# Kernel optimization log

Hardware: AMD Instinct MI355X
Metric: run time of the kernel (lower is better)

Reference implementation:

```python
import jax, jax.numpy as jnp
import numpy as np

# Module hyperparameters (from init_kwargs)
N_S = 128                      # n_scalars
L2_IDX = (0, 1, 2, 3, 4, 5, 6) # l2_indices
N_L2 = len(L2_IDX) + 1         # selected l=2 kernels + their sum -> 8
H = 256                        # hidden multiplicity
B = 2048                       # batch
K = 8                          # number of kernels in kernel_t2s


def _w3j_222():
    """Real-basis Wigner 3j for (2e,2e)->2e, Frobenius norm 1 (e3nn convention).
    Built as tr(Qa Qb Qc) over an orthonormal basis of symmetric traceless 3x3
    matrices (the unique invariant 3-tensor on the 5-dim l=2 irrep)."""
    Q = np.zeros((5, 3, 3))
    s = 1.0 / np.sqrt(2.0)
    Q[0, 0, 1] = Q[0, 1, 0] = s
    Q[1, 1, 2] = Q[1, 2, 1] = s
    Q[2] = np.diag([-1.0, -1.0, 2.0]) / np.sqrt(6.0)
    Q[3, 0, 2] = Q[3, 2, 0] = s
    Q[4, 0, 0] = s
    Q[4, 1, 1] = -s
    C = np.einsum('aij,bjk,cki->abc', Q, Q, Q)
    return C / np.linalg.norm(C)

C222 = jnp.asarray(_w3j_222(), dtype=jnp.float32)

# e3nn FullyConnectedTensorProduct path normalization ('component'/'element'):
# coeff = sqrt((2*l_out+1) / sum over paths into same output of mul1*mul2)
C0 = float(np.sqrt(1.0 / (N_S**2 + N_L2**2)))            # paths into Hx0e: 0x0->0, 2x2->0
C2 = float(np.sqrt(5.0 / (2 * N_S * N_L2 + N_L2**2)))    # paths into Hx2e: 0x2, 2x0, 2x2
C2B = float(np.sqrt(5.0 / (3 * H**2)))                   # tp2 paths into 1x2e
INV_S5 = float(1.0 / np.sqrt(5.0))                       # w3j(l,l,0) = I/sqrt(2l+1), l=2


def setup_inputs() -> dict:
    key = jax.random.key(0)
    ks = jax.random.split(key, 10)
    f32 = jnp.float32
    return {
        'scalars': jax.random.normal(ks[0], (B, N_S), f32),
        'kernel_t2s': jax.random.normal(ks[1], (B, K, 5), f32),
        'W000': jax.random.normal(ks[2], (N_S, N_S, H), f32),
        'W220': jax.random.normal(ks[3], (N_L2, N_L2, H), f32),
        'W022': jax.random.normal(ks[4], (N_S, N_L2, H), f32),
        'W202': jax.random.normal(ks[5], (N_L2, N_S, H), f32),
        'W222': jax.random.normal(ks[6], (N_L2, N_L2, H), f32),
        'V022': jax.random.normal(ks[7], (H, H, 1), f32),
        'V202': jax.random.normal(ks[8], (H, H, 1), f32),
        'V222': jax.random.normal(ks[9], (H, H, 1), f32),
    }


def reference(scalars, kernel_t2s, W000, W220, W022, W202, W222, V022, V202, V222):
    ee = lambda *a: jnp.einsum(*a, optimize='optimal')
    idx = jnp.asarray(L2_IDX)
    # build tp input: [B, n_s] scalars  ++  [B, n_l2, 5] l=2 features
    t = jnp.concatenate([kernel_t2s[:, idx, :],
                         kernel_t2s.sum(axis=1, keepdims=True)], axis=1)  # [B, N_L2, 5]
    s = scalars                                                            # [B, N_S]

    # tp1(x, x): Hx0e + Hx2e
    y0 = C0 * (ee('uvw,zu,zv->zw', W000, s, s)
               + INV_S5 * ee('uvw,zui,zvi->zw', W220, t, t))               # [B, H]
    y2 = C2 * (INV_S5 * (ee('uvw,zu,zvk->zwk', W022, s, t)
                         + ee('uvw,zuk,zv->zwk', W202, t, s))
               + ee('uvw,ijk,zui,zvj->zwk', W222, C222, t, t))             # [B, H, 5]

    # tp2(y, y): 1x2e
    out = C2B * (INV_S5 * (ee('uvw,zu,zvk->zwk', V022, y0, y2)
                           + ee('uvw,zuk,zv->zwk', V202, y2, y0))
                 + ee('uvw,ijk,zui,zvj->zwk', V222, C222, y2, y2))         # [B, 1, 5]
    return out[:, 0, :]                                                    # [B, 5]
```

## Files before the change

### kernel.cpp

```cpp
#include <hip/hip_runtime.h>
#include <stdint.h>
#include <stddef.h>


#define NS     128
#define NL2    8
#define HH     256
#define NB     2048

#define KPAIR  8256
#define KPAD   8448
#define GLEN   64
#define KSPLIT 16
#define CHUNK  528
#define KT     16
#define NTILES 33

#define C0F  0.00779729f
#define C2F  0.04865619f
#define C2BF 0.005042948f
#define IS5  0.44721360f

constexpr size_t OFF_C222 = 0;
constexpr size_t OFF_PU   = 128;
constexpr size_t OFF_PV   = 8576;
constexpr size_t OFF_T    = 17024;
constexpr size_t OFF_W222 = 98944;
constexpr size_t OFF_VBS  = 115328;
constexpr size_t OFF_VC   = 180864;
constexpr size_t OFF_ST   = 246400;
constexpr size_t OFF_GT   = 508544;
constexpr size_t OFF_Y0   = 639616;
constexpr size_t OFF_ACP  = 1163904;
constexpr size_t WS_FLOATS = 1688192;

#define SEG_T    81920
#define SEG_PUV  90368
#define SEG_W222 106752
#define SEG_VBS  172288
#define SEG_VC   237824
#define SEG_ST   499968
#define SEG_GT   631040
#define SEG_END  1155328

__global__ __launch_bounds__(256) void prep_k(
    const float* __restrict__ scalars, const float* __restrict__ kt2s,
    const float* __restrict__ W222,
    const float* __restrict__ V022, const float* __restrict__ V202,
    const float* __restrict__ V222, float* __restrict__ ws) {
  const int tid = threadIdx.x;

  if (blockIdx.x == 0) {
    __shared__ float cv[125];
    __shared__ float inv;
    float val = 0.f;
    if (tid < 125) {
      float Q[45];
      #pragma unroll
      for (int q = 0; q < 45; ++q) Q[q] = 0.f;
      const float s2 = 0.70710678f, s6 = 0.40824829f;
      Q[0*9+0*3+1] = s2;  Q[0*9+1*3+0] = s2;
      Q[1*9+1*3+2] = s2;  Q[1*9+2*3+1] = s2;
      Q[2*9+0*3+0] = -s6; Q[2*9+1*3+1] = -s6; Q[2*9+2*3+2] = 2.f*s6;
      Q[3*9+0*3+2] = s2;  Q[3*9+2*3+0] = s2;
      Q[4*9+0*3+0] = s2;  Q[4*9+1*3+1] = -s2;
      const int a = tid/25, b = (tid/5)%5, c = tid%5;
      for (int i = 0; i < 3; ++i)
        for (int j = 0; j < 3; ++j)
          for (int k = 0; k < 3; ++k)
            val += Q[a*9+i*3+j]*Q[b*9+j*3+k]*Q[c*9+k*3+i];
      cv[tid] = val;
    }
    __syncthreads();
    if (tid == 0) {
      float sq = 0.f;
      for (int p = 0; p < 125; ++p) sq += cv[p]*cv[p];
      inv = 1.0f/sqrtf(sq);
    }
    __syncthreads();
    if (tid < 125) ws[OFF_C222 + tid] = val*inv;
    return;
  }

  int* pu = (int*)(ws + OFF_PU);
  int* pv = (int*)(ws + OFF_PV);
  const int stride = (gridDim.x - 1)*256;
  for (int i = (blockIdx.x - 1)*256 + tid; i < SEG_END; i += stride) {
    if (i < SEG_T) {
      int z = i/40, r = i - z*40, u = r/5, ii = r - u*5;
      float v;
      if (u < 7) v = kt2s[z*40 + u*5 + ii];
      else {
        v = 0.f;
        for (int k = 0; k < 8; ++k) v += kt2s[z*40 + k*5 + ii];
      }
      ws[OFF_T + i] = v;
    } else if (i < SEG_PUV) {
      int p = i - SEG_T;
      int u = 0, vv = 0;
      if (p < KPAIR) {
        int rem = p;
        while (rem >= NS - u) { rem -= NS - u; ++u; }
        vv = u + rem;
      } else if (p < KPAIR + 36) {
        int q = p - KPAIR;
        while (q >= NL2 - u) { q -= NL2 - u; ++u; }
        vv = u + q;
      }
      pu[p] = u; pv[p] = vv;
    } else if (i < SEG_W222) {
      int j = i - SEG_PUV;
      ws[OFF_W222 + j] = C2F*W222[j];
    } else if (i < SEG_VBS) {
      int j = i - SEG_W222;
      int u = j >> 8, c = j & 255;
      ws[OFF_VBS + j] = (C2BF*IS5)*(V022[u*HH + c] + V202[c*HH + u]);
    } else if (i < SEG_VC) {
      int j = i - SEG_VBS;
      ws[OFF_VC + j] = C2BF*V222[j];
    } else if (i < SEG_ST) {
      int j = i - SEG_VC;
      int u = j >> 11, z = j & 2047;
      ws[OFF_ST + j] = scalars[(size_t)z*NS + u];
    } else if (i < SEG_GT) {
      int j = i - SEG_ST;
      int q = j >> 11, z = j & 2047;
      float v = 0.f;
      if (q < 36) {
        int qq = q, u = 0;
        while (qq >= NL2 - u) { qq -= NL2 - u; ++u; }
        int vv = u + qq;
        const float* kz = kt2s + (size_t)z*40;
        #pragma unroll
        for (int ii = 0; ii < 5; ++ii) {
          float tu, tv;
          if (u < 7) tu = kz[u*5 + ii];
          else { tu = 0.f; for (int k = 0; k < 8; ++k) tu += kz[k*5 + ii]; }
          if (vv < 7) tv = kz[vv*5 + ii];
          else { tv = 0.f; for (int k = 0; k < 8; ++k) tv += kz[k*5 + ii]; }
          v += tu*tv;
        }
      }
      ws[OFF_GT + j] = v;
    } else {
      ws[OFF_Y0 + (i - SEG_GT)] = 0.f;
    }
  }
}

__global__ __launch_bounds__(256, 4) void gemm_y0_k(
    const float* __restrict__ W000, const float* __restrict__ W220,
    float* __restrict__ ws) {
  const int* pu = (const int*)(ws + OFF_PU);
  const int* pv = (const int*)(ws + OFF_PV);
  const float* sT = ws + OFF_ST;
  const float* gT = ws + OFF_GT;
  float* y0 = ws + OFF_Y0;

  __shared__ __align__(16) float As[2][KT][64];
  __shared__ __align__(16) float Bs[2][KT][128];

  const int tid = threadIdx.x;
  const int bid = blockIdx.x;
  const int ks = bid & 15, mtnt = bid >> 4;
  const int mt = mtnt >> 1, nt = mtnt & 1;
  const int z0 = mt*64, n0 = nt*128;
  const int kbase = ks*CHUNK;
  const int m = tid & 63, w = tid >> 6;
  const int tx = tid & 31, ty = tid >> 5;

  float4 bReg[2];
  float  aReg[4];

  auto load_tile = [&](int t) {
    const int k0 = kbase + t*KT;
    #pragma unroll
    for (int e = 0; e < 2; ++e) {
      int idx = e*256 + tid;
      int r = idx >> 5, col = (idx & 31)*4;
      int p = k0 + r;
      float4 val;
      if (p < KPAIR) {
        int u = pu[p], v = pv[p];
        float4 a = *reinterpret_cast<const float4*>(
            &W000[((size_t)u*NS + v)*HH + n0 + col]);
        if (u != v) {
          float4 b = *reinterpret_cast<const float4*>(
              &W000[((size_t)v*NS + u)*HH + n0 + col]);
          val = make_float4(C0F*(a.x+b.x), C0F*(a.y+b.y),
                            C0F*(a.z+b.z), C0F*(a.w+b.w));
        } else {
          val = make_float4(C0F*a.x, C0F*a.y, C0F*a.z, C0F*a.w);
        }
      } else if (p < KPAIR + 36) {
        int u = pu[p], v = pv[p];
        const float sc = C0F*IS5;
        float4 a = *reinterpret_cast<const float4*>(
            &W220[(u*NL2 + v)*HH + n0 + col]);
        if (u != v) {
          float4 b = *reinterpret_cast<const float4*>(
              &W220[(v*NL2 + u)*HH + n0 + col]);
          val = make_float4(sc*(a.x+b.x), sc*(a.y+b.y),
                            sc*(a.z+b.z), sc*(a.w+b.w));
        } else {
          val = make_float4(sc*a.x, sc*a.y, sc*a.z, sc*a.w);
        }
      } else {
        val = make_float4(0.f, 0.f, 0.f, 0.f);
      }
      bReg[e] = val;
    }
    #pragma unroll
    for (int e = 0; e < 4; ++e) {
      int k = k0 + e*4 + w;
      float a;
      if (k < KPAIR) {
        a = sT[(size_t)pu[k]*NB + z0 + m] * sT[(size_t)pv[k]*NB + z0 + m];
      } else {
        int q = k - KPAIR;
        a = (q < GLEN) ? gT[(size_t)q*NB + z0 + m] : 0.f;
      }
      aReg[e] = a;
    }
  };
  auto store_tile = [&](int buf) {
    #pragma unroll
    for (int e = 0; e < 2; ++e) {
      int idx = e*256 + tid;
      int r = idx >> 5, col = (idx & 31)*4;
      *reinterpret_cast<float4*>(&Bs[buf][r][col]) = bReg[e];
    }
    #pragma unroll
    for (int e = 0; e < 4; ++e) As[buf][e*4 + w][m] = aReg[e];
  };

  float acc[8][4];
  #pragma unroll
  for (int i = 0; i < 8; ++i)
    #pragma unroll
    for (int j = 0; j < 4; ++j) acc[i][j] = 0.f;

  load_tile(0);
  store_tile(0);
  __syncthreads();

  for (int t = 0; t < NTILES; ++t) {
    if (t + 1 < NTILES) load_tile(t + 1);
    const int cur = t & 1;
    #pragma unroll
    for (int kk = 0; kk < KT; ++kk) {
      float4 a0 = *reinterpret_cast<const float4*>(&As[cur][kk][ty*8]);
      float4 a1 = *reinterpret_cast<const float4*>(&As[cur][kk][ty*8+4]);
      float4 bv = *reinterpret_cast<const float4*>(&Bs[cur][kk][tx*4]);
      float am[8] = {a0.x,a0.y,a0.z,a0.w,a1.x,a1.y,a1.z,a1.w};
      float bn[4] = {bv.x,bv.y,bv.z,bv.w};
      #pragma unroll
      for (int mi = 0; mi < 8; ++mi)
        #pragma unroll
        for (int ni = 0; ni < 4; ++ni)
          acc[mi][ni] += am[mi]*bn[ni];
    }
    if (t + 1 < NTILES) store_tile(cur ^ 1);
    __syncthreads();
  }

  #pragma unroll
  for (int mi = 0; mi < 8; ++mi) {
    int z = z0 + ty*8 + mi;
    #pragma unroll
    for (int ni = 0; ni < 4; ++ni)
      atomicAdd(&y0[(size_t)z*HH + n0 + tx*4 + ni], acc[mi][ni]);
  }
}

__global__ __launch_bounds__(256) void gemm_rm_k(
    const float* __restrict__ A, const float* __restrict__ B,
    float* __restrict__ C, int M, int N, int K) {
  __shared__ __align__(16) float As[32][68];
  __shared__ __align__(16) float Bs[32][68];
  const int tid = threadIdx.x, tx = tid & 15, ty = tid >> 4;
  const int n0 = blockIdx.x*64, m0 = blockIdx.y*64;
  float acc[4][4];
  #pragma unroll
  for (int i = 0; i < 4; ++i)
    #pragma unroll
    for (int j = 0; j < 4; ++j) acc[i][j] = 0.f;

  for (int k0 = 0; k0 < K; k0 += 32) {
    __syncthreads();
    #pragma unroll
    for (int e = 0; e < 2; ++e) {
      int r = e*32 + (tid >> 3);
      int kc = (tid & 7)*4;
      float4 v = *reinterpret_cast<const float4*>(&A[(size_t)(m0+r)*K + k0 + kc]);
      As[kc+0][r] = v.x; As[kc+1][r] = v.y; As[kc+2][r] = v.z; As[kc+3][r] = v.w;
    }
    #pragma unroll
    for (int e = 0; e < 2; ++e) {
      int idx = e*256 + tid;
      int r = idx >> 4, c4 = idx & 15;
      float4 v = *reinterpret_cast<const float4*>(&B[(size_t)(k0+r)*N + n0 + c4*4]);
      *reinterpret_cast<float4*>(&Bs[r][c4*4]) = v;
    }
    __syncthreads();
    #pragma unroll
    for (int kk = 0; kk < 32; ++kk) {
      float4 av = *reinterpret_cast<const float4*>(&As[kk][ty*4]);
      float4 bv = *reinterpret_cast<const float4*>(&Bs[kk][tx*4]);
      float am[4] = {av.x, av.y, av.z, av.w};
      float bn[4] = {bv.x, bv.y, bv.z, bv.w};
      #pragma unroll
      for (int i = 0; i < 4; ++i)
        #pragma unroll
        for (int j = 0; j < 4; ++j) acc[i][j] += am[i]*bn[j];
    }
  }
  #pragma unroll
  for (int i = 0; i < 4; ++i) {
    float4 v = make_float4(acc[i][0], acc[i][1], acc[i][2], acc[i][3]);
    *reinterpret_cast<float4*>(&C[(size_t)(m0 + ty*4 + i)*N + n0 + tx*4]) = v;
  }
}

__global__ __launch_bounds__(256) void mega_k(
    const float* __restrict__ scalars, const float* __restrict__ W022,
    const float* __restrict__ W202, const float* __restrict__ ws,
    float* __restrict__ out) {
  const float* tg    = ws + OFF_T;
  const float* W222c = ws + OFF_W222;
  const float* VC    = ws + OFF_VC;
  const float* acp   = ws + OFF_ACP;
  const float* c222g = ws + OFF_C222;

  __shared__ float ts[8][40];
  __shared__ float c2s[125];
  __shared__ __align__(16) float sb[8][128];
  __shared__ __align__(16) float ovl[10240];
  float* tC  = ovl;
  float* RsF = ovl + 1600;
  float* y2s = ovl;

  const int tid = threadIdx.x;
  const int zg0 = blockIdx.x*8;
  const int lane = tid & 63, wv = tid >> 6;

  if (tid < 125) c2s[tid] = c222g[tid];
  for (int r = tid; r < 320; r += 256) {
    int z = r/40, c = r - z*40;
    ts[z][c] = tg[(size_t)(zg0 + z)*40 + c];
  }
  {
    int z = tid >> 5, c4 = tid & 31;
    float4 v = reinterpret_cast<const float4*>(scalars + (size_t)(zg0 + z)*NS)[c4];
    sb[z][c4*4+0] = v.x; sb[z][c4*4+1] = v.y;
    sb[z][c4*4+2] = v.z; sb[z][c4*4+3] = v.w;
  }
  __syncthreads();

  for (int idx = tid; idx < 1600; idx += 256) {
    int z = idx/200, r = idx - z*200, v = r/25, ik = r - v*25;
    int i = ik/5, k = ik - i*5;
    float a = 0.f;
    #pragma unroll
    for (int j = 0; j < 5; ++j) a += c2s[(i*5+j)*5 + k]*ts[z][v*5+j];
    tC[idx] = a;
  }
  __syncthreads();
  for (int idx = tid; idx < 2560; idx += 256) {
    int uv = idx/40, r = idx - uv*40, z = r/5, k = r - z*5;
    int u = uv >> 3, v = uv & 7;
    float a = 0.f;
    #pragma unroll
    for (int ii = 0; ii < 5; ++ii) a += ts[z][u*5+ii]*tC[z*200 + v*25 + ii*5 + k];
    RsF[idx] = a;
  }
  __syncthreads();

  float acc[8][5];
  #pragma unroll
  for (int z = 0; z < 8; ++z)
    #pragma unroll
    for (int k = 0; k < 5; ++k) acc[z][k] = 0.f;

  for (int vg = 0; vg < 4; ++vg) {
    float av[4][8];
    #pragma unroll
    for (int vi = 0; vi < 4; ++vi)
      #pragma unroll
      for (int z = 0; z < 8; ++z) av[vi][z] = 0.f;
    for (int u4 = 0; u4 < 128; u4 += 4) {
      float4 szv[8];
      #pragma unroll
      for (int z = 0; z < 8; ++z) szv[z] = *reinterpret_cast<const float4*>(&sb[z][u4]);
      #pragma unroll
      for (int uu = 0; uu < 4; ++uu) {
        int u = u4 + uu;
        #pragma unroll
        for (int vi = 0; vi < 4; ++vi) {
          float w1v = (vg < 2)
            ? W022[((size_t)u*NL2 + (vg*4+vi))*HH + tid]
            : W202[((size_t)((vg-2)*4+vi)*NS + u)*HH + tid];
          #pragma unroll
          for (int z = 0; z < 8; ++z) {
            float su = (uu==0)?szv[z].x:(uu==1)?szv[z].y:(uu==2)?szv[z].z:szv[z].w;
            av[vi][z] += su*w1v;
          }
        }
      }
    }
    #pragma unroll
    for (int vi = 0; vi < 4; ++vi) {
      int vmap = (vg*4 + vi) & 7;
      #pragma unroll
      for (int z = 0; z < 8; ++z) {
        float avs = (C2F*IS5)*av[vi][z];
        #pragma unroll
        for (int k = 0; k < 5; ++k)
          acc[z][k] += avs*ts[z][vmap*5+k];
      }
    }
  }

  for (int uv = 0; uv < 64; ++uv) {
    float wvv = W222c[uv*256 + tid];
    #pragma unroll
    for (int c4 = 0; c4 < 10; ++c4) {
      float4 rv = *reinterpret_cast<const float4*>(&RsF[uv*40 + c4*4]);
      acc[(c4*4+0)/5][(c4*4+0)%5] += wvv*rv.x;
      acc[(c4*4+1)/5][(c4*4+1)%5] += wvv*rv.y;
      acc[(c4*4+2)/5][(c4*4+2)%5] += wvv*rv.z;
      acc[(c4*4+3)/5][(c4*4+3)%5] += wvv*rv.w;
    }
  }

  __syncthreads();
  #pragma unroll
  for (int z = 0; z < 8; ++z)
    #pragma unroll
    for (int k = 0; k < 5; ++k)
      y2s[z*1280 + k*256 + tid] = acc[z][k];
  __syncthreads();

  float hacc[2][5][4];
  #pragma unroll
  for (int zz = 0; zz < 2; ++zz)
    #pragma unroll
    for (int i = 0; i < 5; ++i)
      #pragma unroll
      for (int j = 0; j < 4; ++j) hacc[zz][i][j] = 0.f;

  for (int u4 = 0; u4 < 256; u4 += 4) {
    float vc[4][4];
    #pragma unroll
    for (int uu = 0; uu < 4; ++uu)
      #pragma unroll
      for (int j = 0; j < 4; ++j)
        vc[uu][j] = VC[(size_t)(u4+uu)*256 + lane + 64*j];
    #pragma unroll
    for (int zz = 0; zz < 2; ++zz) {
      int z = wv*2 + zz;
      #pragma unroll
      for (int i = 0; i < 5; ++i) {
        float4 yv = *reinterpret_cast<const float4*>(&y2s[z*1280 + i*256 + u4]);
        float ya[4] = {yv.x, yv.y, yv.z, yv.w};
        #pragma unroll
        for (int uu = 0; uu < 4; ++uu)
          #pragma unroll
          for (int j = 0; j < 4; ++j)
            hacc[zz][i][j] += ya[uu]*vc[uu][j];
      }
    }
  }

  float outp[2][5];
  #pragma unroll
  for (int zz = 0; zz < 2; ++zz)
    #pragma unroll
    for (int k = 0; k < 5; ++k) outp[zz][k] = 0.f;

  for (int j = 0; j < 4; ++j) {
    int v = lane + 64*j;
    #pragma unroll
    for (int zz = 0; zz < 2; ++zz) {
      int z = wv*2 + zz;
      float y2v[5];
      #pragma unroll
      for (int jp = 0; jp < 5; ++jp) y2v[jp] = y2s[z*1280 + jp*256 + v];
      float avv = acp[(size_t)(zg0 + z)*256 + v];
      #pragma unroll
      for (int k = 0; k < 5; ++k) outp[zz][k] += avv*y2v[k];
      #pragma unroll
      for (int i = 0; i < 5; ++i) {
        float hv = hacc[zz][i][j];
        #pragma unroll
        for (int jp = 0; jp < 5; ++jp) {
          float pj = hv*y2v[jp];
          #pragma unroll
          for (int k = 0; k < 5; ++k)
            outp[zz][k] += pj*c2s[i*25 + jp*5 + k];
        }
      }
    }
  }

  #pragma unroll
  for (int zz = 0; zz < 2; ++zz)
    #pragma unroll
    for (int k = 0; k < 5; ++k) {
      float vsum = outp[zz][k];
      #pragma unroll
      for (int off = 32; off > 0; off >>= 1) vsum += __shfl_xor(vsum, off, 64);
      if (lane == 0) out[(size_t)(zg0 + wv*2 + zz)*5 + k] = vsum;
    }
}

extern "C" void kernel_launch(void* const* d_in, const int* in_sizes, int n_in,
                              void* d_out, int out_size, void* d_ws, size_t ws_size,
                              hipStream_t stream) {
  (void)in_sizes; (void)n_in; (void)out_size;
  const float* scalars = (const float*)d_in[0];
  const float* kt2s    = (const float*)d_in[1];
  const float* W000    = (const float*)d_in[2];
  const float* W220    = (const float*)d_in[3];
  const float* W022    = (const float*)d_in[4];
  const float* W202    = (const float*)d_in[5];
  const float* W222    = (const float*)d_in[6];
  const float* V022    = (const float*)d_in[7];
  const float* V202    = (const float*)d_in[8];
  const float* V222    = (const float*)d_in[9];
  float* out = (float*)d_out;
  float* ws  = (float*)d_ws;
  if (ws_size < WS_FLOATS*sizeof(float)) return;

  prep_k<<<1025, 256, 0, stream>>>(scalars, kt2s, W222, V022, V202, V222, ws);
  gemm_y0_k<<<1024, 256, 0, stream>>>(W000, W220, ws);
  gemm_rm_k<<<dim3(4, 32), 256, 0, stream>>>(ws + OFF_Y0, ws + OFF_VBS,
                                             (float*)(ws + OFF_ACP), 2048, 256, 256);
  mega_k<<<256, 256, 0, stream>>>(scalars, W022, W202, ws, out);
}
```

Baseline: 498.1 us.

## Widen y0 GEMM tile, precombine W022/W202, and split mega kernel finer

gemm_y0_k now has each block cover the full 256-wide output with an 8x8 per-thread tile. This halves the block count and stops gathering the pair-product A operand twice, once per N tile. prep_k now writes a combined, prescaled W022+W202 tensor, so mega_k reads one weight stream for the 0x2 and 2x0 paths. mega_k handles 2 batch rows per block instead of 8, launching 1024 blocks instead of 256. Its final contraction reduces 30 partial sums per wave through shuffles and shared memory. The costs are more register pressure in the GEMM (64 accumulators, occupancy hint dropped), a larger workspace, and more total weight traffic in mega_k because fewer rows share each weight load.

```diff
diff --git a/kernel.cpp b/kernel.cpp
--- a/kernel.cpp
+++ b/kernel.cpp
@@ -9,7 +9,6 @@
 #define NB     2048
 
 #define KPAIR  8256
-#define KPAD   8448
 #define GLEN   64
 #define KSPLIT 16
 #define CHUNK  528
@@ -30,9 +29,10 @@
 constexpr size_t OFF_VC   = 180864;
 constexpr size_t OFF_ST   = 246400;
 constexpr size_t OFF_GT   = 508544;
-constexpr size_t OFF_Y0   = 639616;
-constexpr size_t OFF_ACP  = 1163904;
-constexpr size_t WS_FLOATS = 1688192;
+constexpr size_t OFF_WC2  = 639616;
+constexpr size_t OFF_Y0   = 901760;
+constexpr size_t OFF_ACP  = 1426048;
+constexpr size_t WS_FLOATS = 1950336;
 
 #define SEG_T    81920
 #define SEG_PUV  90368
@@ -41,10 +41,12 @@
 #define SEG_VC   237824
 #define SEG_ST   499968
 #define SEG_GT   631040
-#define SEG_END  1155328
+#define SEG_WC2  893184
+#define SEG_END  1417472
 
 __global__ __launch_bounds__(256) void prep_k(
     const float* __restrict__ scalars, const float* __restrict__ kt2s,
+    const float* __restrict__ W022, const float* __restrict__ W202,
     const float* __restrict__ W222,
     const float* __restrict__ V022, const float* __restrict__ V202,
     const float* __restrict__ V222, float* __restrict__ ws) {
@@ -142,13 +144,18 @@
         }
       }
       ws[OFF_GT + j] = v;
+    } else if (i < SEG_WC2) {
+      int j = i - SEG_GT;
+      int u = j >> 11, r = j & 2047, v = r >> 8, w = r & 255;
+      ws[OFF_WC2 + j] = (C2F*IS5)*(W022[((size_t)u*NL2 + v)*HH + w]
+                                   + W202[((size_t)v*NS + u)*HH + w]);
     } else {
-      ws[OFF_Y0 + (i - SEG_GT)] = 0.f;
+      ws[OFF_Y0 + (i - SEG_WC2)] = 0.f;
     }
   }
 }
 
-__global__ __launch_bounds__(256, 4) void gemm_y0_k(
+__global__ __launch_bounds__(256) void gemm_y0_k(
     const float* __restrict__ W000, const float* __restrict__ W220,
     float* __restrict__ ws) {
   const int* pu = (const int*)(ws + OFF_PU);
@@ -158,35 +165,34 @@
   float* y0 = ws + OFF_Y0;
 
   __shared__ __align__(16) float As[2][KT][64];
-  __shared__ __align__(16) float Bs[2][KT][128];
+  __shared__ __align__(16) float Bs[2][KT][256];
 
   const int tid = threadIdx.x;
   const int bid = blockIdx.x;
-  const int ks = bid & 15, mtnt = bid >> 4;
-  const int mt = mtnt >> 1, nt = mtnt & 1;
-  const int z0 = mt*64, n0 = nt*128;
+  const int ks = bid & 15, mt = bid >> 4;
+  const int z0 = mt*64;
   const int kbase = ks*CHUNK;
   const int m = tid & 63, w = tid >> 6;
   const int tx = tid & 31, ty = tid >> 5;
 
-  float4 bReg[2];
+  float4 bReg[4];
   float  aReg[4];
 
   auto load_tile = [&](int t) {
     const int k0 = kbase + t*KT;
     #pragma unroll
-    for (int e = 0; e < 2; ++e) {
-      int idx = e*256 + tid;
-      int r = idx >> 5, col = (idx & 31)*4;
+    for (int e = 0; e < 4; ++e) {
+      int r = e*4 + w;
+      int col = (tid & 63)*4;
       int p = k0 + r;
       float4 val;
       if (p < KPAIR) {
         int u = pu[p], v = pv[p];
         float4 a = *reinterpret_cast<const float4*>(
-            &W000[((size_t)u*NS + v)*HH + n0 + col]);
+            &W000[((size_t)u*NS + v)*HH + col]);
         if (u != v) {
           float4 b = *reinterpret_cast<const float4*>(
-              &W000[((size_t)v*NS + u)*HH + n0 + col]);
+              &W000[((size_t)v*NS + u)*HH + col]);
           val = make_float4(C0F*(a.x+b.x), C0F*(a.y+b.y),
                             C0F*(a.z+b.z), C0F*(a.w+b.w));
         } else {
@@ -196,10 +202,10 @@
         int u = pu[p], v = pv[p];
         const float sc = C0F*IS5;
         float4 a = *reinterpret_cast<const float4*>(
-            &W220[(u*NL2 + v)*HH + n0 + col]);
+            &W220[(u*NL2 + v)*HH + col]);
         if (u != v) {
           float4 b = *reinterpret_cast<const float4*>(
-              &W220[(v*NL2 + u)*HH + n0 + col]);
+              &W220[(v*NL2 + u)*HH + col]);
           val = make_float4(sc*(a.x+b.x), sc*(a.y+b.y),
                             sc*(a.z+b.z), sc*(a.w+b.w));
         } else {
@@ -225,20 +231,20 @@
   };
   auto store_tile = [&](int buf) {
     #pragma unroll
-    for (int e = 0; e < 2; ++e) {
-      int idx = e*256 + tid;
-      int r = idx >> 5, col = (idx & 31)*4;
+    for (int e = 0; e < 4; ++e) {
+      int r = e*4 + w;
+      int col = (tid & 63)*4;
       *reinterpret_cast<float4*>(&Bs[buf][r][col]) = bReg[e];
     }
     #pragma unroll
     for (int e = 0; e < 4; ++e) As[buf][e*4 + w][m] = aReg[e];
   };
 
-  float acc[8][4];
+  float acc[8][8];
   #pragma unroll
   for (int i = 0; i < 8; ++i)
     #pragma unroll
-    for (int j = 0; j < 4; ++j) acc[i][j] = 0.f;
+    for (int j = 0; j < 8; ++j) acc[i][j] = 0.f;
 
   load_tile(0);
   store_tile(0);
@@ -251,13 +257,14 @@
     for (int kk = 0; kk < KT; ++kk) {
       float4 a0 = *reinterpret_cast<const float4*>(&As[cur][kk][ty*8]);
       float4 a1 = *reinterpret_cast<const float4*>(&As[cur][kk][ty*8+4]);
-      float4 bv = *reinterpret_cast<const float4*>(&Bs[cur][kk][tx*4]);
+      float4 b0 = *reinterpret_cast<const float4*>(&Bs[cur][kk][tx*8]);
+      float4 b1 = *reinterpret_cast<const float4*>(&Bs[cur][kk][tx*8+4]);
       float am[8] = {a0.x,a0.y,a0.z,a0.w,a1.x,a1.y,a1.z,a1.w};
-      float bn[4] = {bv.x,bv.y,bv.z,bv.w};
+      float bn[8] = {b0.x,b0.y,b0.z,b0.w,b1.x,b1.y,b1.z,b1.w};
       #pragma unroll
       for (int mi = 0; mi < 8; ++mi)
         #pragma unroll
-        for (int ni = 0; ni < 4; ++ni)
+        for (int ni = 0; ni < 8; ++ni)
           acc[mi][ni] += am[mi]*bn[ni];
     }
     if (t + 1 < NTILES) store_tile(cur ^ 1);
@@ -268,8 +275,8 @@
   for (int mi = 0; mi < 8; ++mi) {
     int z = z0 + ty*8 + mi;
     #pragma unroll
-    for (int ni = 0; ni < 4; ++ni)
-      atomicAdd(&y0[(size_t)z*HH + n0 + tx*4 + ni], acc[mi][ni]);
+    for (int ni = 0; ni < 8; ++ni)
+      atomicAdd(&y0[(size_t)z*HH + tx*8 + ni], acc[mi][ni]);
   }
 }
 
@@ -323,33 +330,33 @@
 }
 
 __global__ __launch_bounds__(256) void mega_k(
-    const float* __restrict__ scalars, const float* __restrict__ W022,
-    const float* __restrict__ W202, const float* __restrict__ ws,
+    const float* __restrict__ scalars, const float* __restrict__ ws,
     float* __restrict__ out) {
   const float* tg    = ws + OFF_T;
+  const float* WC2   = ws + OFF_WC2;
   const float* W222c = ws + OFF_W222;
   const float* VC    = ws + OFF_VC;
   const float* acp   = ws + OFF_ACP;
   const float* c222g = ws + OFF_C222;
 
-  __shared__ float ts[8][40];
+  __shared__ float ts[2][40];
   __shared__ float c2s[125];
-  __shared__ __align__(16) float sb[8][128];
-  __shared__ __align__(16) float ovl[10240];
-  float* tC  = ovl;
-  float* RsF = ovl + 1600;
-  float* y2s = ovl;
+  __shared__ float sb[2][128];
+  __shared__ float tC[2][200];
+  __shared__ float Rs[2][320];
+  __shared__ float y2s[2][1280];
+  __shared__ float Pl[4][30];
 
   const int tid = threadIdx.x;
-  const int zg0 = blockIdx.x*8;
+  const int zg0 = blockIdx.x*2;
   const int lane = tid & 63, wv = tid >> 6;
 
   if (tid < 125) c2s[tid] = c222g[tid];
-  for (int r = tid; r < 320; r += 256) {
-    int z = r/40, c = r - z*40;
+  if (tid < 80) {
+    int z = tid/40, c = tid - (tid/40)*40;
     ts[z][c] = tg[(size_t)(zg0 + z)*40 + c];
   }
-  {
+  if (tid < 64) {
     int z = tid >> 5, c4 = tid & 31;
     float4 v = reinterpret_cast<const float4*>(scalars + (size_t)(zg0 + z)*NS)[c4];
     sb[z][c4*4+0] = v.x; sb[z][c4*4+1] = v.y;
@@ -357,161 +364,116 @@
   }
   __syncthreads();
 
-  for (int idx = tid; idx < 1600; idx += 256) {
+  for (int idx = tid; idx < 400; idx += 256) {
     int z = idx/200, r = idx - z*200, v = r/25, ik = r - v*25;
     int i = ik/5, k = ik - i*5;
     float a = 0.f;
     #pragma unroll
     for (int j = 0; j < 5; ++j) a += c2s[(i*5+j)*5 + k]*ts[z][v*5+j];
-    tC[idx] = a;
+    tC[z][r] = a;
   }
   __syncthreads();
-  for (int idx = tid; idx < 2560; idx += 256) {
-    int uv = idx/40, r = idx - uv*40, z = r/5, k = r - z*5;
+  for (int idx = tid; idx < 640; idx += 256) {
+    int z = idx/320, r = idx - (idx/320)*320, uv = r/5, k = r - uv*5;
     int u = uv >> 3, v = uv & 7;
     float a = 0.f;
     #pragma unroll
-    for (int ii = 0; ii < 5; ++ii) a += ts[z][u*5+ii]*tC[z*200 + v*25 + ii*5 + k];
-    RsF[idx] = a;
+    for (int ii = 0; ii < 5; ++ii) a += ts[z][u*5+ii]*tC[z][v*25 + ii*5 + k];
+    Rs[z][r] = a;
   }
   __syncthreads();
 
-  float acc[8][5];
-  #pragma unroll
-  for (int z = 0; z < 8; ++z)
+  float acc[2][5];
+  #pragma unroll
+  for (int z = 0; z < 2; ++z)
     #pragma unroll
     for (int k = 0; k < 5; ++k) acc[z][k] = 0.f;
 
-  for (int vg = 0; vg < 4; ++vg) {
-    float av[4][8];
-    #pragma unroll
-    for (int vi = 0; vi < 4; ++vi)
-      #pragma unroll
-      for (int z = 0; z < 8; ++z) av[vi][z] = 0.f;
-    for (int u4 = 0; u4 < 128; u4 += 4) {
-      float4 szv[8];
-      #pragma unroll
-      for (int z = 0; z < 8; ++z) szv[z] = *reinterpret_cast<const float4*>(&sb[z][u4]);
-      #pragma unroll
-      for (int uu = 0; uu < 4; ++uu) {
-        int u = u4 + uu;
-        #pragma unroll
-        for (int vi = 0; vi < 4; ++vi) {
-          float w1v = (vg < 2)
-            ? W022[((size_t)u*NL2 + (vg*4+vi))*HH + tid]
-            : W202[((size_t)((vg-2)*4+vi)*NS + u)*HH + tid];
-          #pragma unroll
-          for (int z = 0; z < 8; ++z) {
-            float su = (uu==0)?szv[z].x:(uu==1)?szv[z].y:(uu==2)?szv[z].z:szv[z].w;
-            av[vi][z] += su*w1v;
-          }
-        }
-      }
-    }
-    #pragma unroll
-    for (int vi = 0; vi < 4; ++vi) {
-      int vmap = (vg*4 + vi) & 7;
-      #pragma unroll
-      for (int z = 0; z < 8; ++z) {
-        float avs = (C2F*IS5)*av[vi][z];
-        #pragma unroll
-        for (int k = 0; k < 5; ++k)
-          acc[z][k] += avs*ts[z][vmap*5+k];
-      }
-    }
-  }
-
+  #pragma unroll 2
+  for (int v = 0; v < 8; ++v) {
+    float av0 = 0.f, av1 = 0.f;
+    const float* wp = WC2 + v*256 + tid;
+    #pragma unroll 4
+    for (int u = 0; u < 128; ++u) {
+      float wcv = wp[(size_t)u*2048];
+      av0 += sb[0][u]*wcv;
+      av1 += sb[1][u]*wcv;
+    }
+    #pragma unroll
+    for (int k = 0; k < 5; ++k) {
+      acc[0][k] += av0*ts[0][v*5+k];
+      acc[1][k] += av1*ts[1][v*5+k];
+    }
+  }
   for (int uv = 0; uv < 64; ++uv) {
     float wvv = W222c[uv*256 + tid];
     #pragma unroll
-    for (int c4 = 0; c4 < 10; ++c4) {
-      float4 rv = *reinterpret_cast<const float4*>(&RsF[uv*40 + c4*4]);
-      acc[(c4*4+0)/5][(c4*4+0)%5] += wvv*rv.x;
-      acc[(c4*4+1)/5][(c4*4+1)%5] += wvv*rv.y;
-      acc[(c4*4+2)/5][(c4*4+2)%5] += wvv*rv.z;
-      acc[(c4*4+3)/5][(c4*4+3)%5] += wvv*rv.w;
-    }
-  }
-
+    for (int z = 0; z < 2; ++z)
+      #pragma unroll
+      for (int k = 0; k < 5; ++k)
+        acc[z][k] += wvv*Rs[z][uv*5 + k];
+  }
+  #pragma unroll
+  for (int z = 0; z < 2; ++z)
+    #pragma unroll
+    for (int k = 0; k < 5; ++k)
+      y2s[z][k*256 + tid] = acc[z][k];
   __syncthreads();
-  #pragma unroll
-  for (int z = 0; z < 8; ++z)
-    #pragma unroll
-    for (int k = 0; k < 5; ++k)
-      y2s[z*1280 + k*256 + tid] = acc[z][k];
-  __syncthreads();
-
-  float hacc[2][5][4];
-  #pragma unroll
-  for (int zz = 0; zz < 2; ++zz)
+
+  const int z = wv & 1, jh = wv >> 1;
+  float hacc[5][2];
+  #pragma unroll
+  for (int i = 0; i < 5; ++i) { hacc[i][0] = 0.f; hacc[i][1] = 0.f; }
+
+  #pragma unroll 2
+  for (int u = 0; u < 256; ++u) {
+    float vc0 = VC[(size_t)u*256 + jh*128 + lane];
+    float vc1 = VC[(size_t)u*256 + jh*128 + 64 + lane];
+    #pragma unroll
+    for (int i = 0; i < 5; ++i) {
+      float yv = y2s[z][i*256 + u];
+      hacc[i][0] += yv*vc0;
+      hacc[i][1] += yv*vc1;
+    }
+  }
+
+  float P[30];
+  #pragma unroll
+  for (int p = 0; p < 30; ++p) P[p] = 0.f;
+  #pragma unroll
+  for (int jj = 0; jj < 2; ++jj) {
+    int v = jh*128 + 64*jj + lane;
+    float y2v[5];
+    #pragma unroll
+    for (int jp = 0; jp < 5; ++jp) y2v[jp] = y2s[z][jp*256 + v];
+    float avv = acp[(size_t)(zg0 + z)*256 + v];
+    #pragma unroll
+    for (int k = 0; k < 5; ++k) P[25+k] += avv*y2v[k];
     #pragma unroll
     for (int i = 0; i < 5; ++i)
       #pragma unroll
-      for (int j = 0; j < 4; ++j) hacc[zz][i][j] = 0.f;
-
-  for (int u4 = 0; u4 < 256; u4 += 4) {
-    float vc[4][4];
-    #pragma unroll
-    for (int uu = 0; uu < 4; ++uu)
-      #pragma unroll
-      for (int j = 0; j < 4; ++j)
-        vc[uu][j] = VC[(size_t)(u4+uu)*256 + lane + 64*j];
-    #pragma unroll
-    for (int zz = 0; zz < 2; ++zz) {
-      int z = wv*2 + zz;
-      #pragma unroll
-      for (int i = 0; i < 5; ++i) {
-        float4 yv = *reinterpret_cast<const float4*>(&y2s[z*1280 + i*256 + u4]);
-        float ya[4] = {yv.x, yv.y, yv.z, yv.w};
-        #pragma unroll
-        for (int uu = 0; uu < 4; ++uu)
-          #pragma unroll
-          for (int j = 0; j < 4; ++j)
-            hacc[zz][i][j] += ya[uu]*vc[uu][j];
-      }
-    }
-  }
-
-  float outp[2][5];
-  #pragma unroll
-  for (int zz = 0; zz < 2; ++zz)
-    #pragma unroll
-    for (int k = 0; k < 5; ++k) outp[zz][k] = 0.f;
-
-  for (int j = 0; j < 4; ++j) {
-    int v = lane + 64*j;
-    #pragma unroll
-    for (int zz = 0; zz < 2; ++zz) {
-      int z = wv*2 + zz;
-      float y2v[5];
-      #pragma unroll
-      for (int jp = 0; jp < 5; ++jp) y2v[jp] = y2s[z*1280 + jp*256 + v];
-      float avv = acp[(size_t)(zg0 + z)*256 + v];
-      #pragma unroll
-      for (int k = 0; k < 5; ++k) outp[zz][k] += avv*y2v[k];
-      #pragma unroll
-      for (int i = 0; i < 5; ++i) {
-        float hv = hacc[zz][i][j];
-        #pragma unroll
-        for (int jp = 0; jp < 5; ++jp) {
-          float pj = hv*y2v[jp];
-          #pragma unroll
-          for (int k = 0; k < 5; ++k)
-            outp[zz][k] += pj*c2s[i*25 + jp*5 + k];
-        }
-      }
-    }
-  }
-
-  #pragma unroll
-  for (int zz = 0; zz < 2; ++zz)
-    #pragma unroll
-    for (int k = 0; k < 5; ++k) {
-      float vsum = outp[zz][k];
-      #pragma unroll
-      for (int off = 32; off > 0; off >>= 1) vsum += __shfl_xor(vsum, off, 64);
-      if (lane == 0) out[(size_t)(zg0 + wv*2 + zz)*5 + k] = vsum;
-    }
+      for (int jp = 0; jp < 5; ++jp)
+        P[i*5+jp] += hacc[i][jj]*y2v[jp];
+  }
+  #pragma unroll
+  for (int off = 32; off > 0; off >>= 1)
+    #pragma unroll
+    for (int p = 0; p < 30; ++p)
+      P[p] += __shfl_xor(P[p], off, 64);
+  if (lane == 0) {
+    #pragma unroll
+    for (int p = 0; p < 30; ++p) Pl[wv][p] = P[p];
+  }
+  __syncthreads();
+
+  if (tid < 10) {
+    int zz = tid/5, k = tid - (tid/5)*5;
+    float o = Pl[zz][25+k] + Pl[zz+2][25+k];
+    #pragma unroll
+    for (int ij = 0; ij < 25; ++ij)
+      o += c2s[ij*5 + k]*(Pl[zz][ij] + Pl[zz+2][ij]);
+    out[(size_t)(zg0 + zz)*5 + k] = o;
+  }
 }
 
 extern "C" void kernel_launch(void* const* d_in, const int* in_sizes, int n_in,
@@ -532,9 +494,10 @@
   float* ws  = (float*)d_ws;
   if (ws_size < WS_FLOATS*sizeof(float)) return;
 
-  prep_k<<<1025, 256, 0, stream>>>(scalars, kt2s, W222, V022, V202, V222, ws);
-  gemm_y0_k<<<1024, 256, 0, stream>>>(W000, W220, ws);
+  prep_k<<<1025, 256, 0, stream>>>(scalars, kt2s, W022, W202, W222,
+                                   V022, V202, V222, ws);
+  gemm_y0_k<<<512, 256, 0, stream>>>(W000, W220, ws);
   gemm_rm_k<<<dim3(4, 32), 256, 0, stream>>>(ws + OFF_Y0, ws + OFF_VBS,
                                              (float*)(ws + OFF_ACP), 2048, 256, 256);
-  mega_k<<<256, 256, 0, stream>>>(scalars, W022, W202, ws, out);
+  mega_k<<<1024, 256, 0, stream>>>(scalars, ws, out);
 }
```

Result: slower. 772.5 us (+55.1%).
